# Performance work log

Measured on AMD Instinct MI355X. Metric: run time of the kernel, lower is better.

## Reference

```python
import jax, jax.numpy as jnp
import numpy as np

EPS_NORM = 1e-12  # F.normalize eps
EPS_LN = 1e-5     # nn.LayerNorm default eps

def _l2norm(x, axis=-1):
    n = jnp.linalg.norm(x, axis=axis, keepdims=True)
    return x / jnp.maximum(n, EPS_NORM)

def setup_inputs() -> dict:
    key = jax.random.key(0)
    k1, k2 = jax.random.split(key)
    n, b, d = 2048, 8, 1024
    x = jax.random.normal(k1, (n, b, d), dtype=jnp.float32)
    embed = jax.random.normal(k2, (n, d), dtype=jnp.float32)  # xavier-like
    gamma = jnp.ones((d,), dtype=jnp.float32)
    beta = jnp.zeros((d,), dtype=jnp.float32)
    return {"x": x, "embed": embed, "gamma": gamma, "beta": beta}

def reference(x, embed, gamma, beta):
    # x: [n, b, d]; embed: [n, d] (broadcast over batch, as in .expand)
    wn = _l2norm(embed)          # [n, d]
    xn = _l2norm(x)              # [n, b, d]
    scores = jnp.einsum('nd,mbd->nbm', wn, xn)    # cosine similarities
    weights = jax.nn.softmax(scores, axis=-1)     # [n, b, m]
    out = jnp.einsum('nbm,mbd->nbd', weights, x)  # weighted sum of raw input
    # dropout is identity in eval mode
    y = out + x
    mu = jnp.mean(y, axis=-1, keepdims=True)
    var = jnp.var(y, axis=-1, keepdims=True)
    return (y - mu) * jax.lax.rsqrt(var + EPS_LN) * gamma + beta
```

## Files before the change

kernel.cpp:

```cpp
#include <hip/hip_runtime.h>
#include <hip/hip_bf16.h>

typedef float f4 __attribute__((ext_vector_type(4)));
typedef int i32x4 __attribute__((ext_vector_type(4)));
typedef int i32x8 __attribute__((ext_vector_type(8)));
typedef unsigned char u8x16 __attribute__((ext_vector_type(16)));

#define N_TOK 2048
#define BATCH 8
#define DIM   1024

static __device__ __forceinline__ unsigned int pk4_fp8(float a, float b, float c, float d) {
  unsigned int v = 0;
  v = __builtin_amdgcn_cvt_pk_fp8_f32(a, b, v, false);
  v = __builtin_amdgcn_cvt_pk_fp8_f32(c, d, v, true);
  return v;
}
static __device__ __forceinline__ unsigned char fp8_1(float a) {
  return (unsigned char)(__builtin_amdgcn_cvt_pk_fp8_f32(a, a, 0, false) & 0xFF);
}
static __device__ __forceinline__ unsigned short f2bf(float f) {
  unsigned int b = __float_as_uint(f);
  b += 0x7FFFu + ((b >> 16) & 1u);
  return (unsigned short)(b >> 16);
}
static __device__ __forceinline__ float bf2f(unsigned short u) {
  return __uint_as_float(((unsigned int)u) << 16);
}

static __device__ __forceinline__ void gld16(const void* g, void* lds) {
  __builtin_amdgcn_global_load_lds(
      (const __attribute__((address_space(1))) unsigned int*)g,
      (__attribute__((address_space(3))) unsigned int*)lds, 16, 0, 0);
}

static __device__ __forceinline__ void stage_tile(const unsigned char* g, size_t ldb,
                                                  unsigned char* lds, int w, int l) {
  const int rgrp = l >> 3;
  const int srcb = (((l & 7) ^ rgrp) << 4);
  #pragma unroll
  for (int gi = 0; gi < 4; ++gi) {
    int rb = (gi * 4 + w) * 8;
    gld16(g + (size_t)(rb + rgrp) * ldb + srcb, lds + (gi * 4 + w) * 1024);
  }
}

static __device__ __forceinline__ i32x8 fragld32(const unsigned char* lds, int row, int kb) {
  const unsigned char* base = lds + row * 128;
  const int swz = (row & 7) << 4;
  const i32x4 lo = *(const i32x4*)(base + (kb ^ swz));
  const i32x4 hi = *(const i32x4*)(base + ((kb + 16) ^ swz));
  i32x8 r;
  r[0] = lo[0]; r[1] = lo[1]; r[2] = lo[2]; r[3] = lo[3];
  r[4] = hi[0]; r[5] = hi[1]; r[6] = hi[2]; r[7] = hi[3];
  return r;
}

static __device__ __forceinline__ void gemm_mx(unsigned char* sA, unsigned char* sB,
    const unsigned char* Ab, size_t lda, const unsigned char* Bb, size_t ldb,
    int nk, int w, int l, int wr, int wc, f4 acc[4][4]) {
  for (int kk = 0; kk < nk; ++kk) {
    stage_tile(Ab + (size_t)kk * 128, lda, sA, w, l);
    stage_tile(Bb + (size_t)kk * 128, ldb, sB, w, l);
    __syncthreads();
    const int kb = (l >> 4) * 32;
    i32x8 af[4], bf[4];
    #pragma unroll
    for (int i = 0; i < 4; ++i)
      af[i] = fragld32(sA, wr * 64 + i * 16 + (l & 15), kb);
    #pragma unroll
    for (int j = 0; j < 4; ++j)
      bf[j] = fragld32(sB, wc * 64 + j * 16 + (l & 15), kb);
    #pragma unroll
    for (int i = 0; i < 4; ++i)
      #pragma unroll
      for (int j = 0; j < 4; ++j)
        acc[i][j] = __builtin_amdgcn_mfma_scale_f32_16x16x128_f8f6f4(
            af[i], bf[j], acc[i][j], 0, 0, 0, 0x7F7F7F7F, 0, 0x7F7F7F7F);
    __syncthreads();
  }
}


static __device__ __forceinline__ float block_reduce_sum(float v, volatile float* sb, int t) {
  #pragma unroll
  for (int o = 32; o; o >>= 1) v += __shfl_xor(v, o);
  if ((t & 63) == 0) sb[t >> 6] = v;
  __syncthreads();
  float r = sb[0] + sb[1] + sb[2] + sb[3];
  __syncthreads();
  return r;
}

__global__ __launch_bounds__(256) void prep_wn(const float* __restrict__ e,
                                               unsigned char* __restrict__ wn,
                                               float* __restrict__ winv) {
  __shared__ float sb[4];
  const int n = blockIdx.x, t = threadIdx.x;
  const float4 v = *(const float4*)(e + (size_t)n * DIM + t * 4);
  float ss = v.x * v.x + v.y * v.y + v.z * v.z + v.w * v.w;
  ss = block_reduce_sum(ss, sb, t);
  if (t == 0) winv[n] = rsqrtf(fmaxf(ss, 1e-24f));
  *(unsigned int*)(wn + (size_t)n * DIM + t * 4) = pk4_fp8(v.x, v.y, v.z, v.w);
}

__global__ __launch_bounds__(256) void prep_x(const float* __restrict__ x,
    unsigned char* __restrict__ xr8, unsigned char* __restrict__ XT,
    float* __restrict__ sspart) {
  __shared__ unsigned char tile[64][72];
  const int t = threadIdx.x;
  const int m0 = blockIdx.x * 64, d0 = blockIdx.y * 64, b = blockIdx.z;
  {
    const int ml = t >> 2, dc = (t & 3) * 16;
    const float* row = x + ((size_t)(m0 + ml) * BATCH + b) * DIM + d0 + dc;
    union { unsigned int u[4]; u8x16 v; } pk;
    float ssp = 0.0f;
    #pragma unroll
    for (int i = 0; i < 4; ++i) {
      float4 v = *(const float4*)(row + i * 4);
      ssp += v.x * v.x + v.y * v.y + v.z * v.z + v.w * v.w;
      pk.u[i] = pk4_fp8(v.x, v.y, v.z, v.w);
    }
    *(u8x16*)(xr8 + ((size_t)b * N_TOK + m0 + ml) * DIM + d0 + dc) = pk.v;
    *(u8x16*)&tile[ml][dc] = pk.v;
    ssp += __shfl_xor(ssp, 1);
    ssp += __shfl_xor(ssp, 2);
    if ((t & 3) == 0)
      sspart[((size_t)b * N_TOK + m0 + ml) * 16 + (d0 >> 6)] = ssp;
  }
  __syncthreads();
  {
    const int dl = t >> 2, mc = (t & 3) * 16;
    union { unsigned char c[16]; u8x16 v; } o;
    #pragma unroll
    for (int ii = 0; ii < 16; ++ii) o.c[ii] = tile[mc + ii][dl];
    *(u8x16*)(XT + ((size_t)b * DIM + d0 + dl) * (size_t)N_TOK + m0 + mc) = o.v;
  }
}

__global__ __launch_bounds__(256) void prep_xinv(const float* __restrict__ sspart,
                                                 float* __restrict__ xinv) {
  const int i = blockIdx.x * 256 + threadIdx.x;
  const float* p = sspart + (size_t)i * 16;
  float s = 0.0f;
  #pragma unroll
  for (int k = 0; k < 16; ++k) s += p[k];
  xinv[i] = rsqrtf(fmaxf(s, 1e-24f));
}


__global__ __launch_bounds__(256, 3) void kA(
    const unsigned char* __restrict__ wn, const unsigned char* __restrict__ xr8,
    const float* __restrict__ winv, const float* __restrict__ xinv,
    unsigned char* __restrict__ Pp, float* __restrict__ pden, int Mc, int c0) {
  __shared__ __align__(16) unsigned char sA[16384];
  __shared__ __align__(16) unsigned char sB[16384];
  __shared__ float pd[128][2];
  __shared__ float winv_s[128], xinv_s[128];

  const int t = threadIdx.x, l = t & 63, w = t >> 6;
  const int wr = w >> 1, wc = w & 1;

  const int gy = Mc >> 7;
  const int nwg = 16 * gy * 8;
  const int lin = blockIdx.x + 16 * (blockIdx.y + gy * blockIdx.z);
  const int wg = (lin & 7) * (nwg >> 3) + (lin >> 3);
  const int xx = wg & 15, yy = (wg >> 4) % gy, zz = (wg >> 4) / gy;

  const int q0 = xx * 128;
  const int m0l = yy * 128;
  const int b = zz;
  const int m0g = c0 + m0l;

  if (t < 128) winv_s[t] = winv[q0 + t];
  else         xinv_s[t - 128] = xinv[b * N_TOK + m0g + (t - 128)];

  f4 acc[4][4];
  #pragma unroll
  for (int i = 0; i < 4; ++i)
    #pragma unroll
    for (int j = 0; j < 4; ++j) acc[i][j] = (f4)0.0f;

  gemm_mx(sA, sB,
          wn + (size_t)q0 * DIM, DIM,
          xr8 + ((size_t)b * N_TOK + m0g) * DIM, DIM,
          DIM / 128, w, l, wr, wc, acc);

  float ra[4][4];
  #pragma unroll
  for (int i = 0; i < 4; ++i)
    #pragma unroll
    for (int e = 0; e < 4; ++e) ra[i][e] = 0.0f;

  #pragma unroll
  for (int j = 0; j < 4; ++j) {
    const int cl = wc * 64 + j * 16 + (l & 15);
    const float xv = xinv_s[cl];
    #pragma unroll
    for (int i = 0; i < 4; ++i)
      #pragma unroll
      for (int e = 0; e < 4; ++e) {
        const int row = wr * 64 + i * 16 + (l >> 4) * 4 + e;
        const float p = __expf(acc[i][j][e] * winv_s[row] * xv);
        ra[i][e] += p;
        Pp[((size_t)b * N_TOK + q0 + row) * (size_t)Mc + m0l + cl] = fp8_1(p);
      }
  }
  #pragma unroll
  for (int i = 0; i < 4; ++i)
    #pragma unroll
    for (int e = 0; e < 4; ++e) {
      float s = ra[i][e];
      s += __shfl_xor(s, 1); s += __shfl_xor(s, 2);
      s += __shfl_xor(s, 4); s += __shfl_xor(s, 8);
      if ((l & 15) == 0) pd[wr * 64 + i * 16 + (l >> 4) * 4 + e][wc] = s;
    }
  __syncthreads();
  if (t < 128)
    pden[((size_t)b * N_TOK + q0 + t) * 16 + (c0 >> 7) + yy] = pd[t][0] + pd[t][1];
}


template <int ACC, int FINAL, int YBF>
__global__ __launch_bounds__(256, 3) void kB(const unsigned char* __restrict__ Pp,
    const unsigned char* __restrict__ XT, const float* __restrict__ x,
    const float* __restrict__ pden, float* __restrict__ out,
    unsigned short* __restrict__ ybf, int Mc, int c0) {
  __shared__ __align__(16) unsigned char sA[16384];
  __shared__ __align__(16) unsigned char sB[16384];
  __shared__ float rden_s[128];

  const int t = threadIdx.x, l = t & 63, w = t >> 6;
  const int wr = w >> 1, wc = w & 1;

  const int lin = blockIdx.x + 16 * (blockIdx.y + 8 * blockIdx.z);
  const int wg = (lin & 7) * 128 + (lin >> 3);
  const int q0 = (wg & 15) * 128;
  const int d0 = ((wg >> 4) & 7) * 128;
  const int b = wg >> 7;

  f4 acc[4][4];
  #pragma unroll
  for (int i = 0; i < 4; ++i)
    #pragma unroll
    for (int j = 0; j < 4; ++j) acc[i][j] = (f4)0.0f;

  gemm_mx(sA, sB,
          Pp + ((size_t)b * N_TOK + q0) * (size_t)Mc, (size_t)Mc,
          XT + (((size_t)b * DIM + d0) * (size_t)N_TOK + c0), (size_t)N_TOK,
          Mc / 128, w, l, wr, wc, acc);

  if (FINAL) {
    if (t < 128) {
      const float* pp = pden + ((size_t)b * N_TOK + q0 + t) * 16;
      float s = 0.0f;
      #pragma unroll
      for (int i = 0; i < 16; ++i) s += pp[i];
      rden_s[t] = 1.0f / s;
    }
    __syncthreads();
  }

  #pragma unroll
  for (int j = 0; j < 4; ++j) {
    const int cc = d0 + wc * 64 + j * 16 + (l & 15);
    #pragma unroll
    for (int i = 0; i < 4; ++i)
      #pragma unroll
      for (int e = 0; e < 4; ++e) {
        const int rl = wr * 64 + i * 16 + (l >> 4) * 4 + e;
        const size_t oi = (size_t)(q0 + rl) * (BATCH * DIM) + (size_t)b * DIM + cc;
        float v = acc[i][j][e];
        if (ACC) v += out[oi];
        if (FINAL) {
          v = v * rden_s[rl] + x[oi];
          if (YBF) { ybf[oi] = f2bf(v); continue; }
        }
        out[oi] = v;
      }
  }
}


template <int YBF>
__global__ __launch_bounds__(256) void kLN(const float* __restrict__ gamma,
    const float* __restrict__ beta, const unsigned short* __restrict__ ybf,
    float* __restrict__ out) {
  __shared__ float sb[8];
  const int r = blockIdx.x;
  const int t = threadIdx.x;

  const size_t base = (size_t)r * DIM;
  float y0, y1, y2, y3;
  if (YBF) {
    const ushort4 u = *(const ushort4*)(ybf + base + t * 4);
    y0 = bf2f(u.x); y1 = bf2f(u.y); y2 = bf2f(u.z); y3 = bf2f(u.w);
  } else {
    const float4 y4 = *(const float4*)(out + base + t * 4);
    y0 = y4.x; y1 = y4.y; y2 = y4.z; y3 = y4.w;
  }

  float s1 = y0 + y1 + y2 + y3;
  float s2 = y0 * y0 + y1 * y1 + y2 * y2 + y3 * y3;
  #pragma unroll
  for (int o = 32; o; o >>= 1) { s1 += __shfl_xor(s1, o); s2 += __shfl_xor(s2, o); }
  if ((t & 63) == 0) { sb[t >> 6] = s1; sb[4 + (t >> 6)] = s2; }
  __syncthreads();
  s1 = sb[0] + sb[1] + sb[2] + sb[3];
  s2 = sb[4] + sb[5] + sb[6] + sb[7];

  const float mean = s1 * (1.0f / DIM);
  const float var = s2 * (1.0f / DIM) - mean * mean;
  const float rstd = rsqrtf(var + 1e-5f);

  const float4 g4 = *(const float4*)(gamma + t * 4);
  const float4 b4 = *(const float4*)(beta + t * 4);
  float4 rr;
  rr.x = (y0 - mean) * rstd * g4.x + b4.x;
  rr.y = (y1 - mean) * rstd * g4.y + b4.y;
  rr.z = (y2 - mean) * rstd * g4.z + b4.z;
  rr.w = (y3 - mean) * rstd * g4.w + b4.w;
  *(float4*)(out + base + t * 4) = rr;
}


extern "C" void kernel_launch(void* const* d_in, const int* in_sizes, int n_in,
                              void* d_out, int out_size, void* d_ws, size_t ws_size,
                              hipStream_t stream) {
  (void)in_sizes; (void)n_in; (void)out_size;
  const float* x     = (const float*)d_in[0];
  const float* embed = (const float*)d_in[1];
  const float* gamma = (const float*)d_in[2];
  const float* beta  = (const float*)d_in[3];
  float* out = (float*)d_out;

  size_t off = 0;
  char* ws = (char*)d_ws;
  auto take = [&](size_t bytes) { char* p = ws + off; off += bytes; return p; };
  unsigned char* XT   = (unsigned char*)take((size_t)BATCH * DIM * N_TOK);
  unsigned char* xr8  = (unsigned char*)take((size_t)BATCH * N_TOK * DIM);
  unsigned char* wn8  = (unsigned char*)take((size_t)N_TOK * DIM);
  float* winv   = (float*)take((size_t)N_TOK * 4);
  float* sspart = (float*)take((size_t)BATCH * N_TOK * 16 * 4);
  float* xinv   = (float*)take((size_t)BATCH * N_TOK * 4);
  float* pden   = (float*)take((size_t)BATCH * N_TOK * 16 * 4);
  const size_t fixed = off;

  int Mc = 2048;
  while (Mc > 128 && fixed + (size_t)BATCH * N_TOK * Mc > ws_size) Mc >>= 1;
  unsigned char* Pp = (unsigned char*)take((size_t)BATCH * N_TOK * Mc);

  const size_t ybf_bytes = (size_t)N_TOK * BATCH * DIM * 2;
  const int use_ybf = (off + ybf_bytes <= ws_size) ? 1 : 0;
  unsigned short* ybf = use_ybf ? (unsigned short*)take(ybf_bytes) : (unsigned short*)out;

  prep_wn<<<N_TOK, 256, 0, stream>>>(embed, wn8, winv);
  prep_x<<<dim3(N_TOK / 64, DIM / 64, BATCH), 256, 0, stream>>>(x, xr8, XT, sspart);
  prep_xinv<<<(N_TOK * BATCH) / 256, 256, 0, stream>>>(sspart, xinv);

  const int nchunk = N_TOK / Mc;
  for (int ci = 0; ci < nchunk; ++ci) {
    const int c0 = ci * Mc;
    kA<<<dim3(16, Mc / 128, BATCH), 256, 0, stream>>>(wn8, xr8, winv, xinv, Pp, pden, Mc, c0);
    const bool first = (ci == 0), last = (ci == nchunk - 1);
    const dim3 gB(16, 8, BATCH);
    if (last) {
      if (use_ybf) {
        if (first) kB<0, 1, 1><<<gB, 256, 0, stream>>>(Pp, XT, x, pden, out, ybf, Mc, c0);
        else       kB<1, 1, 1><<<gB, 256, 0, stream>>>(Pp, XT, x, pden, out, ybf, Mc, c0);
      } else {
        if (first) kB<0, 1, 0><<<gB, 256, 0, stream>>>(Pp, XT, x, pden, out, ybf, Mc, c0);
        else       kB<1, 1, 0><<<gB, 256, 0, stream>>>(Pp, XT, x, pden, out, ybf, Mc, c0);
      }
    } else {
      if (first) kB<0, 0, 0><<<gB, 256, 0, stream>>>(Pp, XT, x, pden, out, ybf, Mc, c0);
      else       kB<1, 0, 0><<<gB, 256, 0, stream>>>(Pp, XT, x, pden, out, ybf, Mc, c0);
    }
  }
  if (use_ybf) kLN<1><<<N_TOK * BATCH, 256, 0, stream>>>(gamma, beta, ybf, out);
  else         kLN<0><<<N_TOK * BATCH, 256, 0, stream>>>(gamma, beta, ybf, out);
}
```

Before: 148.4 us.

## Move residual add into LayerNorm using bf16 copy of x; remap kB tile order

The residual add of x moves out of the GEMM epilogue and into the LayerNorm kernel. prep_x now also writes a bf16 copy of x, so kB no longer reads fp32 x with its scattered epilogue pattern, and kLN reads x as bf16 instead of fp32. kB's workgroup-to-tile mapping is also changed so d-tiles vary fastest within a q block. The cost is an extra 32MB bf16 write in prep_x and extra workspace, plus some precision loss from rounding x to bf16 before the add.

```diff
diff --git a/kernel.cpp b/kernel.cpp
--- a/kernel.cpp
+++ b/kernel.cpp
@@ -5,6 +5,7 @@
 typedef int i32x4 __attribute__((ext_vector_type(4)));
 typedef int i32x8 __attribute__((ext_vector_type(8)));
 typedef unsigned char u8x16 __attribute__((ext_vector_type(16)));
+typedef unsigned short u16x8 __attribute__((ext_vector_type(8)));
 
 #define N_TOK 2048
 #define BATCH 8
@@ -104,24 +105,35 @@
   *(unsigned int*)(wn + (size_t)n * DIM + t * 4) = pk4_fp8(v.x, v.y, v.z, v.w);
 }
 
+template <int XBF>
 __global__ __launch_bounds__(256) void prep_x(const float* __restrict__ x,
     unsigned char* __restrict__ xr8, unsigned char* __restrict__ XT,
-    float* __restrict__ sspart) {
+    unsigned short* __restrict__ xbf, float* __restrict__ sspart) {
   __shared__ unsigned char tile[64][72];
   const int t = threadIdx.x;
   const int m0 = blockIdx.x * 64, d0 = blockIdx.y * 64, b = blockIdx.z;
   {
     const int ml = t >> 2, dc = (t & 3) * 16;
-    const float* row = x + ((size_t)(m0 + ml) * BATCH + b) * DIM + d0 + dc;
+    const size_t roff = ((size_t)(m0 + ml) * BATCH + b) * DIM + d0 + dc;
+    const float* row = x + roff;
     union { unsigned int u[4]; u8x16 v; } pk;
+    union { unsigned short u[16]; u16x8 v[2]; } bfp;
     float ssp = 0.0f;
     #pragma unroll
     for (int i = 0; i < 4; ++i) {
       float4 v = *(const float4*)(row + i * 4);
       ssp += v.x * v.x + v.y * v.y + v.z * v.z + v.w * v.w;
       pk.u[i] = pk4_fp8(v.x, v.y, v.z, v.w);
+      if (XBF) {
+        bfp.u[i * 4 + 0] = f2bf(v.x); bfp.u[i * 4 + 1] = f2bf(v.y);
+        bfp.u[i * 4 + 2] = f2bf(v.z); bfp.u[i * 4 + 3] = f2bf(v.w);
+      }
     }
     *(u8x16*)(xr8 + ((size_t)b * N_TOK + m0 + ml) * DIM + d0 + dc) = pk.v;
+    if (XBF) {
+      *(u16x8*)(xbf + roff) = bfp.v[0];
+      *(u16x8*)(xbf + roff + 8) = bfp.v[1];
+    }
     *(u8x16*)&tile[ml][dc] = pk.v;
     ssp += __shfl_xor(ssp, 1);
     ssp += __shfl_xor(ssp, 2);
@@ -221,11 +233,10 @@
 }
 
 
-template <int ACC, int FINAL, int YBF>
+template <int ACC, int FINAL, int OBF>
 __global__ __launch_bounds__(256, 3) void kB(const unsigned char* __restrict__ Pp,
-    const unsigned char* __restrict__ XT, const float* __restrict__ x,
-    const float* __restrict__ pden, float* __restrict__ out,
-    unsigned short* __restrict__ ybf, int Mc, int c0) {
+    const unsigned char* __restrict__ XT, const float* __restrict__ pden,
+    float* __restrict__ of32, unsigned short* __restrict__ obf, int Mc, int c0) {
   __shared__ __align__(16) unsigned char sA[16384];
   __shared__ __align__(16) unsigned char sB[16384];
   __shared__ float rden_s[128];
@@ -235,8 +246,9 @@
 
   const int lin = blockIdx.x + 16 * (blockIdx.y + 8 * blockIdx.z);
   const int wg = (lin & 7) * 128 + (lin >> 3);
-  const int q0 = (wg & 15) * 128;
-  const int d0 = ((wg >> 4) & 7) * 128;
+  const int s = wg & 127;
+  const int d0 = (s & 7) * 128;
+  const int q0 = (s >> 3) * 128;
   const int b = wg >> 7;
 
   f4 acc[4][4];
@@ -253,10 +265,10 @@
   if (FINAL) {
     if (t < 128) {
       const float* pp = pden + ((size_t)b * N_TOK + q0 + t) * 16;
-      float s = 0.0f;
+      float ss = 0.0f;
       #pragma unroll
-      for (int i = 0; i < 16; ++i) s += pp[i];
-      rden_s[t] = 1.0f / s;
+      for (int i = 0; i < 16; ++i) ss += pp[i];
+      rden_s[t] = 1.0f / ss;
     }
     __syncthreads();
   }
@@ -271,34 +283,43 @@
         const int rl = wr * 64 + i * 16 + (l >> 4) * 4 + e;
         const size_t oi = (size_t)(q0 + rl) * (BATCH * DIM) + (size_t)b * DIM + cc;
         float v = acc[i][j][e];
-        if (ACC) v += out[oi];
+        if (ACC) v += of32[oi];
         if (FINAL) {
-          v = v * rden_s[rl] + x[oi];
-          if (YBF) { ybf[oi] = f2bf(v); continue; }
+          v *= rden_s[rl];
+          if (OBF) { obf[oi] = f2bf(v); continue; }
         }
-        out[oi] = v;
+        of32[oi] = v;
       }
   }
 }
 
 
-template <int YBF>
+template <int OBF, int XBF>
 __global__ __launch_bounds__(256) void kLN(const float* __restrict__ gamma,
-    const float* __restrict__ beta, const unsigned short* __restrict__ ybf,
-    float* __restrict__ out) {
+    const float* __restrict__ beta, const unsigned short* __restrict__ obf,
+    const float* __restrict__ of32, const unsigned short* __restrict__ xbf,
+    const float* __restrict__ x, float* __restrict__ out) {
   __shared__ float sb[8];
   const int r = blockIdx.x;
   const int t = threadIdx.x;
 
-  const size_t base = (size_t)r * DIM;
-  float y0, y1, y2, y3;
-  if (YBF) {
-    const ushort4 u = *(const ushort4*)(ybf + base + t * 4);
-    y0 = bf2f(u.x); y1 = bf2f(u.y); y2 = bf2f(u.z); y3 = bf2f(u.w);
+  const size_t base = (size_t)r * DIM + t * 4;
+  float o0, o1, o2, o3, x0, x1, x2, x3;
+  if (OBF) {
+    const ushort4 u = *(const ushort4*)(obf + base);
+    o0 = bf2f(u.x); o1 = bf2f(u.y); o2 = bf2f(u.z); o3 = bf2f(u.w);
   } else {
-    const float4 y4 = *(const float4*)(out + base + t * 4);
-    y0 = y4.x; y1 = y4.y; y2 = y4.z; y3 = y4.w;
-  }
+    const float4 o4 = *(const float4*)(of32 + base);
+    o0 = o4.x; o1 = o4.y; o2 = o4.z; o3 = o4.w;
+  }
+  if (XBF) {
+    const ushort4 u = *(const ushort4*)(xbf + base);
+    x0 = bf2f(u.x); x1 = bf2f(u.y); x2 = bf2f(u.z); x3 = bf2f(u.w);
+  } else {
+    const float4 x4 = *(const float4*)(x + base);
+    x0 = x4.x; x1 = x4.y; x2 = x4.z; x3 = x4.w;
+  }
+  const float y0 = o0 + x0, y1 = o1 + x1, y2 = o2 + x2, y3 = o3 + x3;
 
   float s1 = y0 + y1 + y2 + y3;
   float s2 = y0 * y0 + y1 * y1 + y2 * y2 + y3 * y3;
@@ -320,7 +341,7 @@
   rr.y = (y1 - mean) * rstd * g4.y + b4.y;
   rr.z = (y2 - mean) * rstd * g4.z + b4.z;
   rr.w = (y3 - mean) * rstd * g4.w + b4.w;
-  *(float4*)(out + base + t * 4) = rr;
+  *(float4*)(out + (size_t)r * DIM + t * 4) = rr;
 }
 
 
@@ -350,12 +371,17 @@
   while (Mc > 128 && fixed + (size_t)BATCH * N_TOK * Mc > ws_size) Mc >>= 1;
   unsigned char* Pp = (unsigned char*)take((size_t)BATCH * N_TOK * Mc);
 
-  const size_t ybf_bytes = (size_t)N_TOK * BATCH * DIM * 2;
-  const int use_ybf = (off + ybf_bytes <= ws_size) ? 1 : 0;
-  unsigned short* ybf = use_ybf ? (unsigned short*)take(ybf_bytes) : (unsigned short*)out;
+  const size_t half = (size_t)N_TOK * BATCH * DIM * 2;
+  const int use_obf = (off + half <= ws_size) ? 1 : 0;
+  unsigned short* obf = use_obf ? (unsigned short*)take(half) : (unsigned short*)out;
+  const int use_xbf = (off + half <= ws_size) ? 1 : 0;
+  unsigned short* xbf = use_xbf ? (unsigned short*)take(half) : (unsigned short*)out;
 
   prep_wn<<<N_TOK, 256, 0, stream>>>(embed, wn8, winv);
-  prep_x<<<dim3(N_TOK / 64, DIM / 64, BATCH), 256, 0, stream>>>(x, xr8, XT, sspart);
+  if (use_xbf)
+    prep_x<1><<<dim3(N_TOK / 64, DIM / 64, BATCH), 256, 0, stream>>>(x, xr8, XT, xbf, sspart);
+  else
+    prep_x<0><<<dim3(N_TOK / 64, DIM / 64, BATCH), 256, 0, stream>>>(x, xr8, XT, xbf, sspart);
   prep_xinv<<<(N_TOK * BATCH) / 256, 256, 0, stream>>>(sspart, xinv);
 
   const int nchunk = N_TOK / Mc;
@@ -365,18 +391,23 @@
     const bool first = (ci == 0), last = (ci == nchunk - 1);
     const dim3 gB(16, 8, BATCH);
     if (last) {
-      if (use_ybf) {
-        if (first) kB<0, 1, 1><<<gB, 256, 0, stream>>>(Pp, XT, x, pden, out, ybf, Mc, c0);
-        else       kB<1, 1, 1><<<gB, 256, 0, stream>>>(Pp, XT, x, pden, out, ybf, Mc, c0);
+      if (use_obf) {
+        if (first) kB<0, 1, 1><<<gB, 256, 0, stream>>>(Pp, XT, pden, out, obf, Mc, c0);
+        else       kB<1, 1, 1><<<gB, 256, 0, stream>>>(Pp, XT, pden, out, obf, Mc, c0);
       } else {
-        if (first) kB<0, 1, 0><<<gB, 256, 0, stream>>>(Pp, XT, x, pden, out, ybf, Mc, c0);
-        else       kB<1, 1, 0><<<gB, 256, 0, stream>>>(Pp, XT, x, pden, out, ybf, Mc, c0);
+        if (first) kB<0, 1, 0><<<gB, 256, 0, stream>>>(Pp, XT, pden, out, obf, Mc, c0);
+        else       kB<1, 1, 0><<<gB, 256, 0, stream>>>(Pp, XT, pden, out, obf, Mc, c0);
       }
     } else {
-      if (first) kB<0, 0, 0><<<gB, 256, 0, stream>>>(Pp, XT, x, pden, out, ybf, Mc, c0);
-      else       kB<1, 0, 0><<<gB, 256, 0, stream>>>(Pp, XT, x, pden, out, ybf, Mc, c0);
+      if (first) kB<0, 0, 0><<<gB, 256, 0, stream>>>(Pp, XT, pden, out, obf, Mc, c0);
+      else       kB<1, 0, 0><<<gB, 256, 0, stream>>>(Pp, XT, pden, out, obf, Mc, c0);
     }
   }
-  if (use_ybf) kLN<1><<<N_TOK * BATCH, 256, 0, stream>>>(gamma, beta, ybf, out);
-  else         kLN<0><<<N_TOK * BATCH, 256, 0, stream>>>(gamma, beta, ybf, out);
-}
+  if (use_obf) {
+    if (use_xbf) kLN<1, 1><<<N_TOK * BATCH, 256, 0, stream>>>(gamma, beta, obf, out, xbf, x, out);
+    else         kLN<1, 0><<<N_TOK * BATCH, 256, 0, stream>>>(gamma, beta, obf, out, xbf, x, out);
+  } else {
+    if (use_xbf) kLN<0, 1><<<N_TOK * BATCH, 256, 0, stream>>>(gamma, beta, obf, out, xbf, x, out);
+    else         kLN<0, 0><<<N_TOK * BATCH, 256, 0, stream>>>(gamma, beta, obf, out, xbf, x, out);
+  }
+}
```

Result: slower. 155.4 us (+4.7%).
